# Performance work log

Measured on AMD Instinct MI355X. Metric: run time of the kernel, lower is better.

## Reference

```python
import jax, jax.numpy as jnp
import numpy as np

N_HEAD, DK, DV = 16, 64, 64
TEMP = DK ** 0.5
LN_EPS = 1e-5


def setup_inputs() -> dict:
    key = jax.random.key(0)
    ks = jax.random.split(key, 8)
    B, LQ, LK = 8, 1024, 1024
    D1, D2 = 768, 1024
    return {
        'q': jax.random.normal(ks[0], (B, LQ, D1), jnp.float32),
        'k': jax.random.normal(ks[1], (B, LK, D2), jnp.float32),
        'v': jax.random.normal(ks[2], (B, LK, D2), jnp.float32),
        'w_qs': jax.random.normal(ks[3], (D1, N_HEAD * DK), jnp.float32) * 0.02,
        'w_ks': jax.random.normal(ks[4], (D2, N_HEAD * DK), jnp.float32) * 0.02,
        'w_vs': jax.random.normal(ks[5], (D2, N_HEAD * DV), jnp.float32) * 0.02,
        'fc_w': jax.random.normal(ks[6], (N_HEAD * DV, D2), jnp.float32) * 0.02,
        'resid_w': jax.random.normal(ks[7], (D1, N_HEAD * DV), jnp.float32) * 0.02,
        'resid_b': jnp.zeros((N_HEAD * DV,), jnp.float32),
        'ln_gamma': jnp.ones((D2,), jnp.float32),
        'ln_beta': jnp.zeros((D2,), jnp.float32),
    }


def reference(q, k, v, w_qs, w_ks, w_vs, fc_w, resid_w, resid_b, ln_gamma, ln_beta):
    B, LQ, _ = q.shape
    LK = k.shape[1]
    residual = q
    # project and split heads: [B, L, H, d] -> [B, H, L, d]
    Q = (q @ w_qs).reshape(B, LQ, N_HEAD, DK).transpose(0, 2, 1, 3)
    K = (k @ w_ks).reshape(B, LK, N_HEAD, DK).transpose(0, 2, 1, 3)
    V = (v @ w_vs).reshape(B, LK, N_HEAD, DV).transpose(0, 2, 1, 3)
    scores = jnp.einsum('bhqd,bhkd->bhqk', Q / TEMP, K)
    p = jax.nn.softmax(scores, axis=-1)
    # reverse-complement attention (RCA): reverse=True
    p = (1.0 - p) / (LK - 1)
    out = jnp.einsum('bhqk,bhkd->bhqd', p, V)  # dropout is eval-mode identity
    out = out.transpose(0, 2, 1, 3).reshape(B, LQ, N_HEAD * DV)
    out = out @ fc_w
    out = out + (residual @ resid_w + resid_b)
    mean = jnp.mean(out, axis=-1, keepdims=True)
    var = jnp.var(out, axis=-1, keepdims=True)
    out = (out - mean) * jax.lax.rsqrt(var + LN_EPS) * ln_gamma + ln_beta
    return out  # relu=False
```

## Files before the change

### kernel.cpp

```cpp
#include <hip/hip_runtime.h>

typedef __bf16 bf16_t;
typedef __bf16 bf16x8 __attribute__((ext_vector_type(8)));
typedef __bf16 bf16x4 __attribute__((ext_vector_type(4)));
typedef float  f32x4  __attribute__((ext_vector_type(4)));

#if __has_builtin(__builtin_amdgcn_exp2f)
#define EXP2(x) __builtin_amdgcn_exp2f(x)
#else
#define EXP2(x) exp2f(x)
#endif

#define DEVFN __device__ __forceinline__

DEVFN void gl_lds16(void* lds_base, const void* gsrc) {
  __builtin_amdgcn_global_load_lds(
      (const __attribute__((address_space(1))) void*)gsrc,
      (__attribute__((address_space(3))) void*)lds_base, 16, 0, 0);
}

__global__ __launch_bounds__(256) void k_prep(
    const float* __restrict__ q, const float* __restrict__ k, const float* __restrict__ v,
    const float* __restrict__ w_qs, const float* __restrict__ w_ks,
    const float* __restrict__ w_vs, const float* __restrict__ fc_w,
    const float* __restrict__ resid_w,
    bf16_t* __restrict__ qb, bf16_t* __restrict__ kb, bf16_t* __restrict__ vb,
    bf16_t* __restrict__ wqsT, bf16_t* __restrict__ wksT, bf16_t* __restrict__ wvsT,
    bf16_t* __restrict__ fcwT, bf16_t* __restrict__ rswT,
    float* __restrict__ Vs) {
  __shared__ float t[64][65];
  int bid = blockIdx.x;
  if (bid < 1152) {
    const float* w; bf16_t* wt; int K;
    if (bid < 192)      { w = w_qs;    wt = wqsT; K = 768; }
    else if (bid < 448) { w = w_ks;    wt = wksT; K = 1024; bid -= 192; }
    else if (bid < 704) { w = w_vs;    wt = wvsT; K = 1024; bid -= 448; }
    else if (bid < 960) { w = fc_w;    wt = fcwT; K = 1024; bid -= 704; }
    else                { w = resid_w; wt = rswT; K = 768;  bid -= 960; }
    const int bk = (bid >> 4) << 6;
    const int bn = (bid & 15) << 6;
    const int rr = threadIdx.x >> 4;
    const int cc = (threadIdx.x & 15) << 2;
#pragma unroll
    for (int i = 0; i < 4; ++i) {
      int r = i * 16 + rr;
      float4 vv = *reinterpret_cast<const float4*>(&w[(size_t)(bk + r) * 1024 + bn + cc]);
      t[r][cc] = vv.x; t[r][cc + 1] = vv.y; t[r][cc + 2] = vv.z; t[r][cc + 3] = vv.w;
    }
    __syncthreads();
#pragma unroll
    for (int i = 0; i < 4; ++i) {
      int n = i * 16 + rr;
      bf16x4 o;
      o[0] = (bf16_t)t[cc][n];     o[1] = (bf16_t)t[cc + 1][n];
      o[2] = (bf16_t)t[cc + 2][n]; o[3] = (bf16_t)t[cc + 3][n];
      *reinterpret_cast<bf16x4*>(&wt[(size_t)(bn + n) * K + bk + cc]) = o;
    }
    return;
  }
  bid -= 1152;
  if (bid == 0) {
    for (int j = threadIdx.x; j < 8192; j += 256) Vs[j] = 0.f;
  }
  const int NQ = 1572864, NK = 2097152, NT = NQ + 2 * NK;
  int stride = (gridDim.x - 1152) * 256;
  for (int i = bid * 256 + threadIdx.x; i < NT; i += stride) {
    const float* src; bf16_t* dst; int off;
    if (i < NQ)           { src = q; dst = qb; off = i; }
    else if (i < NQ + NK) { src = k; dst = kb; off = i - NQ; }
    else                  { src = v; dst = vb; off = i - NQ - NK; }
    float4 vv = reinterpret_cast<const float4*>(src)[off];
    bf16x4 o;
    o[0] = (bf16_t)vv.x; o[1] = (bf16_t)vv.y; o[2] = (bf16_t)vv.z; o[3] = (bf16_t)vv.w;
    reinterpret_cast<bf16x4*>(dst)[off] = o;
  }
}

DEVFN void gemm_tiles(const bf16_t* __restrict__ A, const bf16_t* __restrict__ Bt,
                      int K, int m0, int n0, bf16_t (*sm)[4096], f32x4 (&acc)[4][4]) {
  const int lane = threadIdx.x & 63;
  const int wv = threadIdx.x >> 6;
  const int wr = (wv >> 1) * 64, wc = (wv & 1) * 64;
  const int lr = lane & 15, lk = lane >> 4;
  const int so0 = wv * 2048 + lane * 16;
  const int so1 = so0 + 1024;
  const int r0 = so0 >> 6, r1 = so1 >> 6;
  const int c0 = ((((so0 >> 4) & 3) ^ ((r0 >> 1) & 3)) << 4);
  const int c1 = ((((so1 >> 4) & 3) ^ ((r1 >> 1) & 3)) << 4);
  const int asw = ((lk ^ ((lr >> 1) & 3)) << 4);
  const char* Apc = (const char*)A;
  const char* Btc = (const char*)Bt;
  f32x4 zro = {0.f, 0.f, 0.f, 0.f};
#pragma unroll
  for (int i = 0; i < 4; ++i)
#pragma unroll
    for (int j = 0; j < 4; ++j) acc[i][j] = zro;

  const int nk = K >> 5;
  auto stage = [&](int buf, int t) {
    gl_lds16((char*)sm[buf] + wv * 2048,        Apc + ((size_t)(m0 + r0) * K + t * 32) * 2 + c0);
    gl_lds16((char*)sm[buf] + wv * 2048 + 1024, Apc + ((size_t)(m0 + r1) * K + t * 32) * 2 + c1);
    gl_lds16((char*)sm[2 + buf] + wv * 2048,        Btc + ((size_t)(n0 + r0) * K + t * 32) * 2 + c0);
    gl_lds16((char*)sm[2 + buf] + wv * 2048 + 1024, Btc + ((size_t)(n0 + r1) * K + t * 32) * 2 + c1);
  };
  stage(0, 0);
  __syncthreads();
  for (int t = 0; t < nk; ++t) {
    const int cur = t & 1;
    if (t + 1 < nk) stage(cur ^ 1, t + 1);
    const char* AsB = (const char*)sm[cur];
    const char* BsB = (const char*)sm[2 + cur];
    bf16x8 af[4], bfr[4];
#pragma unroll
    for (int i = 0; i < 4; ++i)
      af[i] = *(const bf16x8*)(AsB + (wr + i * 16 + lr) * 64 + asw);
#pragma unroll
    for (int j = 0; j < 4; ++j)
      bfr[j] = *(const bf16x8*)(BsB + (wc + j * 16 + lr) * 64 + asw);
#pragma unroll
    for (int i = 0; i < 4; ++i)
#pragma unroll
      for (int j = 0; j < 4; ++j)
        acc[i][j] = __builtin_amdgcn_mfma_f32_16x16x32_bf16(af[i], bfr[j], acc[i][j], 0, 0, 0);
    __syncthreads();
  }
}

__global__ __launch_bounds__(256) void k_gemm_proj(
    const bf16_t* __restrict__ qb, const bf16_t* __restrict__ wqsT, bf16_t* __restrict__ Qp,
    const bf16_t* __restrict__ kb, const bf16_t* __restrict__ wksT, bf16_t* __restrict__ Kp,
    const bf16_t* __restrict__ vb, const bf16_t* __restrict__ wvsT, bf16_t* __restrict__ Vt,
    float* __restrict__ Vsum, float qscale) {
  __shared__ bf16_t sm[4][4096];
  const int bid = blockIdx.x;
  const int route = bid >> 9;
  const int sbid = bid & 511;
  const int wg = (sbid & 7) * 64 + (sbid >> 3);
  const int tn = 8;
  const int m0 = (wg / tn) << 7;
  const int n0 = (wg % tn) << 7;
  const int lane = threadIdx.x & 63;
  const int wv = threadIdx.x >> 6;
  const int wr = (wv >> 1) * 64, wc = (wv & 1) * 64;
  const int lr = lane & 15, lk = lane >> 4;
  f32x4 acc[4][4];

  if (route == 0) {
    gemm_tiles(vb, wvsT, 1024, m0, n0, sm, acc);
    const int b = m0 >> 10;
    const int h0 = n0 >> 6;
    const int kt0 = (m0 & 1023) >> 6;
    const int h_local = wc >> 6, kt_local = wr >> 6;
    char* tl = (char*)sm + (h_local * 2 + kt_local) * 8192;
#pragma unroll
    for (int i = 0; i < 4; ++i) {
      const int kvl = i * 16 + lk * 4;
      const int csel = kvl >> 3;
      const int hoff = (kvl & 7) * 2;
#pragma unroll
      for (int j = 0; j < 4; ++j) {
        const int d = j * 16 + lr;
        bf16x4 pw;
#pragma unroll
        for (int r = 0; r < 4; ++r) pw[r] = (bf16_t)acc[i][j][r];
        *reinterpret_cast<bf16x4*>(tl + d * 128 + ((csel ^ (d & 7)) << 4) + hoff) = pw;
      }
    }
    {
      const size_t gbase = (size_t)(b * 16 + h0 + h_local) * 131072 +
                           (size_t)(kt0 + kt_local) * 8192;
#pragma unroll
      for (int it = 0; it < 8; ++it)
        *reinterpret_cast<uint4*>((char*)Vt + gbase + it * 1024 + lane * 16) =
            *reinterpret_cast<const uint4*>(tl + it * 1024 + lane * 16);
    }
    const int h = h0 + h_local;
#pragma unroll
    for (int j = 0; j < 4; ++j) {
      float s = 0.f;
#pragma unroll
      for (int i = 0; i < 4; ++i)
#pragma unroll
        for (int r = 0; r < 4; ++r) s += acc[i][j][r];
      s += __shfl_xor(s, 16, 64);
      s += __shfl_xor(s, 32, 64);
      if (lane < 16)
        atomicAdd(&Vsum[(b * 16 + h) * 64 + j * 16 + lane], s);
    }
  } else if (route == 1) {
    gemm_tiles(kb, wksT, 1024, m0, n0, sm, acc);
#pragma unroll
    for (int i = 0; i < 4; ++i)
#pragma unroll
      for (int j = 0; j < 4; ++j)
#pragma unroll
        for (int r = 0; r < 4; ++r)
          Kp[(size_t)(m0 + wr + i * 16 + lk * 4 + r) * 1024 + n0 + wc + j * 16 + lr] =
              (bf16_t)acc[i][j][r];
  } else {
    gemm_tiles(qb, wqsT, 768, m0, n0, sm, acc);
#pragma unroll
    for (int i = 0; i < 4; ++i)
#pragma unroll
      for (int j = 0; j < 4; ++j)
#pragma unroll
        for (int r = 0; r < 4; ++r)
          Qp[(size_t)(m0 + wr + i * 16 + lk * 4 + r) * 1024 + n0 + wc + j * 16 + lr] =
              (bf16_t)(acc[i][j][r] * qscale);
  }
}

__global__ __launch_bounds__(256) void k_gemm_final(
    const bf16_t* __restrict__ A1, const bf16_t* __restrict__ B1t, int K1,
    const bf16_t* __restrict__ A2, const bf16_t* __restrict__ B2t, int K2,
    const float* __restrict__ bias, bf16_t* __restrict__ Y, int N) {
  __shared__ bf16_t sm[4][4096];
  const int bpx = gridDim.x >> 3;
  const int wg = (blockIdx.x & 7) * bpx + (blockIdx.x >> 3);
  const int tn = N >> 7;
  const int m0 = (wg / tn) << 7;
  const int n0 = (wg % tn) << 7;
  const int lane = threadIdx.x & 63;
  const int wv = threadIdx.x >> 6;
  const int wr = (wv >> 1) * 64, wc = (wv & 1) * 64;
  const int lr = lane & 15, lk = lane >> 4;
  const int so0 = wv * 2048 + lane * 16;
  const int so1 = so0 + 1024;
  const int r0 = so0 >> 6, r1 = so1 >> 6;
  const int c0 = ((((so0 >> 4) & 3) ^ ((r0 >> 1) & 3)) << 4);
  const int c1 = ((((so1 >> 4) & 3) ^ ((r1 >> 1) & 3)) << 4);
  const int asw = ((lk ^ ((lr >> 1) & 3)) << 4);
  f32x4 zro = {0.f, 0.f, 0.f, 0.f};
  f32x4 acc[4][4];
#pragma unroll
  for (int i = 0; i < 4; ++i)
#pragma unroll
    for (int j = 0; j < 4; ++j) acc[i][j] = zro;

  const int nk1 = K1 >> 5;
  const int nkt = (K1 + K2) >> 5;
  auto stage = [&](int buf, int t) {
    const char* Apc; const char* Btc; int K, tt;
    if (t < nk1) { Apc = (const char*)A1; Btc = (const char*)B1t; K = K1; tt = t; }
    else         { Apc = (const char*)A2; Btc = (const char*)B2t; K = K2; tt = t - nk1; }
    gl_lds16((char*)sm[buf] + wv * 2048,        Apc + ((size_t)(m0 + r0) * K + tt * 32) * 2 + c0);
    gl_lds16((char*)sm[buf] + wv * 2048 + 1024, Apc + ((size_t)(m0 + r1) * K + tt * 32) * 2 + c1);
    gl_lds16((char*)sm[2 + buf] + wv * 2048,        Btc + ((size_t)(n0 + r0) * K + tt * 32) * 2 + c0);
    gl_lds16((char*)sm[2 + buf] + wv * 2048 + 1024, Btc + ((size_t)(n0 + r1) * K + tt * 32) * 2 + c1);
  };
  stage(0, 0);
  __syncthreads();
  for (int t = 0; t < nkt; ++t) {
    const int cur = t & 1;
    if (t + 1 < nkt) stage(cur ^ 1, t + 1);
    const char* AsB = (const char*)sm[cur];
    const char* BsB = (const char*)sm[2 + cur];
    bf16x8 af[4], bfr[4];
#pragma unroll
    for (int i = 0; i < 4; ++i)
      af[i] = *(const bf16x8*)(AsB + (wr + i * 16 + lr) * 64 + asw);
#pragma unroll
    for (int j = 0; j < 4; ++j)
      bfr[j] = *(const bf16x8*)(BsB + (wc + j * 16 + lr) * 64 + asw);
#pragma unroll
    for (int i = 0; i < 4; ++i)
#pragma unroll
      for (int j = 0; j < 4; ++j)
        acc[i][j] = __builtin_amdgcn_mfma_f32_16x16x32_bf16(af[i], bfr[j], acc[i][j], 0, 0, 0);
    __syncthreads();
  }
#pragma unroll
  for (int i = 0; i < 4; ++i)
#pragma unroll
    for (int j = 0; j < 4; ++j) {
      float bv = bias[n0 + wc + j * 16 + lr];
#pragma unroll
      for (int r = 0; r < 4; ++r)
        Y[(size_t)(m0 + wr + i * 16 + lk * 4 + r) * N + n0 + wc + j * 16 + lr] =
            (bf16_t)(acc[i][j][r] + bv);
    }
}

__global__ __launch_bounds__(1024) void k_attn(
    const bf16_t* __restrict__ Qp, const bf16_t* __restrict__ Kp,
    const bf16_t* __restrict__ Vt, const float* __restrict__ Vsum,
    bf16_t* __restrict__ Aout) {
  const int bid = blockIdx.x;
  const int wgid = (bid & 7) * 32 + (bid >> 3);
  const int qg = wgid & 1;
  const int bh = wgid >> 1;
  const int b = bh >> 4, h = bh & 15;
  __shared__ bf16_t Ks[2][4096];
  __shared__ bf16_t Vs[2][4096];
  const int tid = threadIdx.x;
  const int lane = tid & 63;
  const int wv = tid >> 6;
  const int lr = lane & 15, lk = lane >> 4;
  const int stb = (wv >> 2) * 2;
  const int wrow = (wv & 3) * 16;

  const int o = (tid & 511) * 16;
  const int row = o >> 7;
  const int sc = ((((o >> 4) & 7) ^ (row & 7)) << 4);
  const int srow = (row & 0x23) | ((row & 0x0C) << 1) | ((row & 0x10) >> 2);
  const bool isK = tid < 512;

  const char* Ksrc  = (const char*)(Kp + ((size_t)(b * 1024 + srow)) * 1024 + h * 64) + sc;
  const char* Vtile = (const char*)Vt + (size_t)bh * 131072 + o;
  const char* gsrc   = isK ? Ksrc : Vtile;
  const size_t gstep = isK ? (size_t)131072 : (size_t)8192;
  char* l0 = isK ? ((char*)&Ks[0][0] + o) : ((char*)&Vs[0][0] + o);
  char* l1 = isK ? ((char*)&Ks[1][0] + o) : ((char*)&Vs[1][0] + o);

  gl_lds16(l0, gsrc);

  bf16x8 qa[2][2];
#pragma unroll
  for (int stl = 0; stl < 2; ++stl) {
    const char* qsrc = (const char*)(Qp +
        ((size_t)(b * 1024 + qg * 512 + (stb + stl) * 64 + wrow + lr)) * 1024 + h * 64);
    qa[stl][0] = *(const bf16x8*)(qsrc + lk * 16);
    qa[stl][1] = *(const bf16x8*)(qsrc + 64 + lk * 16);
  }
  __syncthreads();

  const int kb0 = lr * 128 + ((lk ^ (lr & 7)) << 4);
  const int kb1 = lr * 128 + (((4 + lk) ^ (lr & 7)) << 4);

  f32x4 zro = {0.f, 0.f, 0.f, 0.f};
  f32x4 oacc[2][4];
  f32x4 sum[2];
#pragma unroll
  for (int stl = 0; stl < 2; ++stl) {
    sum[stl] = zro;
#pragma unroll
    for (int g = 0; g < 4; ++g) oacc[stl][g] = zro;
  }
  bf16x8 ones8;
#pragma unroll
  for (int j = 0; j < 8; ++j) ones8[j] = (bf16_t)1.0f;

  for (int kt = 0; kt < 16; ++kt) {
    const int cur = kt & 1;
    const char* KsB = (const char*)&Ks[cur][0];
    const char* VsB = (const char*)&Vs[cur][0];
    if (kt < 15)
      gl_lds16(cur ? l0 : l1, gsrc + (size_t)(kt + 1) * gstep);

    f32x4 sacc[2][4];
#pragma unroll
    for (int stl = 0; stl < 2; ++stl)
#pragma unroll
      for (int g = 0; g < 4; ++g) sacc[stl][g] = zro;
    {
      bf16x8 kf[4];
#pragma unroll
      for (int g = 0; g < 4; ++g) kf[g] = *(const bf16x8*)(KsB + kb0 + g * 2048);
#pragma unroll
      for (int stl = 0; stl < 2; ++stl)
#pragma unroll
        for (int g = 0; g < 4; ++g)
          sacc[stl][g] = __builtin_amdgcn_mfma_f32_16x16x32_bf16(kf[g], qa[stl][0], sacc[stl][g], 0, 0, 0);
#pragma unroll
      for (int g = 0; g < 4; ++g) kf[g] = *(const bf16x8*)(KsB + kb1 + g * 2048);
#pragma unroll
      for (int stl = 0; stl < 2; ++stl)
#pragma unroll
        for (int g = 0; g < 4; ++g)
          sacc[stl][g] = __builtin_amdgcn_mfma_f32_16x16x32_bf16(kf[g], qa[stl][1], sacc[stl][g], 0, 0, 0);
    }

    bf16x8 pa[2][2];
#pragma unroll
    for (int stl = 0; stl < 2; ++stl)
#pragma unroll
      for (int c = 0; c < 2; ++c) {
        bf16x8 pw;
#pragma unroll
        for (int r = 0; r < 4; ++r) {
          pw[r]     = (bf16_t)EXP2(sacc[stl][2 * c][r]);
          pw[4 + r] = (bf16_t)EXP2(sacc[stl][2 * c + 1][r]);
        }
        pa[stl][c] = pw;
      }

#pragma unroll
    for (int c = 0; c < 2; ++c) {
      const int vb = (c == 0) ? kb0 : kb1;
      bf16x8 vf[4];
#pragma unroll
      for (int gd = 0; gd < 4; ++gd)
        vf[gd] = *(const bf16x8*)(VsB + vb + gd * 2048);
#pragma unroll
      for (int stl = 0; stl < 2; ++stl) {
        sum[stl] = __builtin_amdgcn_mfma_f32_16x16x32_bf16(pa[stl][c], ones8, sum[stl], 0, 0, 0);
#pragma unroll
        for (int gd = 0; gd < 4; ++gd)
          oacc[stl][gd] = __builtin_amdgcn_mfma_f32_16x16x32_bf16(pa[stl][c], vf[gd], oacc[stl][gd], 0, 0, 0);
      }
    }
    __syncthreads();
  }

  float vs_d[4];
#pragma unroll
  for (int gd = 0; gd < 4; ++gd) vs_d[gd] = Vsum[bh * 64 + gd * 16 + lr];
#pragma unroll
  for (int stl = 0; stl < 2; ++stl) {
    float inv[4];
#pragma unroll
    for (int r = 0; r < 4; ++r) inv[r] = 1.0f / sum[stl][r];
#pragma unroll
    for (int gd = 0; gd < 4; ++gd)
#pragma unroll
      for (int r = 0; r < 4; ++r) {
        int d = gd * 16 + lr;
        int qrow = qg * 512 + (stb + stl) * 64 + wrow + lk * 4 + r;
        float attnv = oacc[stl][gd][r] * inv[r];
        float val = (vs_d[gd] - attnv) * (1.0f / 1023.0f);
        Aout[((size_t)(b * 1024 + qrow)) * 1024 + h * 64 + d] = (bf16_t)val;
      }
  }
}

__global__ __launch_bounds__(256) void k_ln(
    const bf16_t* __restrict__ Y, const float* __restrict__ gamma,
    const float* __restrict__ beta, float* __restrict__ out) {
  const int row = blockIdx.x, tid = threadIdx.x;
  bf16x4 xv = reinterpret_cast<const bf16x4*>(Y + (size_t)row * 1024)[tid];
  float x0 = (float)xv[0], x1 = (float)xv[1], x2 = (float)xv[2], x3 = (float)xv[3];
  float s = x0 + x1 + x2 + x3;
  float q = x0 * x0 + x1 * x1 + x2 * x2 + x3 * x3;
#pragma unroll
  for (int off = 32; off > 0; off >>= 1) {
    s += __shfl_xor(s, off, 64);
    q += __shfl_xor(q, off, 64);
  }
  __shared__ float ss[4], qs[4];
  if ((tid & 63) == 0) { ss[tid >> 6] = s; qs[tid >> 6] = q; }
  __syncthreads();
  s = ss[0] + ss[1] + ss[2] + ss[3];
  q = qs[0] + qs[1] + qs[2] + qs[3];
  float mean = s * (1.f / 1024.f);
  float var = q * (1.f / 1024.f) - mean * mean;
  float rstd = rsqrtf(var + 1e-5f);
  float4 g = reinterpret_cast<const float4*>(gamma)[tid];
  float4 bt = reinterpret_cast<const float4*>(beta)[tid];
  float4 o;
  o.x = (x0 - mean) * rstd * g.x + bt.x;
  o.y = (x1 - mean) * rstd * g.y + bt.y;
  o.z = (x2 - mean) * rstd * g.z + bt.z;
  o.w = (x3 - mean) * rstd * g.w + bt.w;
  reinterpret_cast<float4*>(out + (size_t)row * 1024)[tid] = o;
}

extern "C" void kernel_launch(void* const* d_in, const int* in_sizes, int n_in,
                              void* d_out, int out_size, void* d_ws, size_t ws_size,
                              hipStream_t stream) {
  (void)in_sizes; (void)n_in; (void)out_size;
  const float* q       = (const float*)d_in[0];
  const float* k       = (const float*)d_in[1];
  const float* v       = (const float*)d_in[2];
  const float* w_qs    = (const float*)d_in[3];
  const float* w_ks    = (const float*)d_in[4];
  const float* w_vs    = (const float*)d_in[5];
  const float* fc_w    = (const float*)d_in[6];
  const float* resid_w = (const float*)d_in[7];
  const float* resid_b = (const float*)d_in[8];
  const float* ln_g    = (const float*)d_in[9];
  const float* ln_b    = (const float*)d_in[10];
  float* out = (float*)d_out;
  char* ws = (char*)d_ws;

  if (ws_size < (size_t)122716160) return;

  bf16_t* qb   = (bf16_t*)(ws + 0);
  bf16_t* kb   = (bf16_t*)(ws + 12582912);
  bf16_t* vb   = (bf16_t*)(ws + 29360128);
  bf16_t* Y    = (bf16_t*)(ws + 12582912);
  bf16_t* wqsT = (bf16_t*)(ws + 46137344);
  bf16_t* wksT = (bf16_t*)(ws + 47710208);
  bf16_t* wvsT = (bf16_t*)(ws + 49807360);
  bf16_t* fcwT = (bf16_t*)(ws + 51904512);
  bf16_t* rswT = (bf16_t*)(ws + 54001664);
  bf16_t* Qp   = (bf16_t*)(ws + 55574528);
  bf16_t* Kp   = (bf16_t*)(ws + 72351744);
  bf16_t* Aout = (bf16_t*)(ws + 89128960);
  bf16_t* VtT  = (bf16_t*)(ws + 105906176);
  float*  Vsm  = (float*)(ws + 122683392);

  k_prep<<<3200, 256, 0, stream>>>(q, k, v, w_qs, w_ks, w_vs, fc_w, resid_w,
                                   qb, kb, vb, wqsT, wksT, wvsT, fcwT, rswT, Vsm);
  k_gemm_proj<<<1536, 256, 0, stream>>>(qb, wqsT, Qp, kb, wksT, Kp, vb, wvsT, VtT,
                                        Vsm, 0.18033688011f);
  k_attn<<<256, 1024, 0, stream>>>(Qp, Kp, VtT, Vsm, Aout);
  k_gemm_final<<<512, 256, 0, stream>>>(Aout, fcwT, 1024, qb, rswT, 768, resid_b, Y, 1024);
  k_ln<<<8192, 256, 0, stream>>>(Y, ln_g, ln_b, out);
}
```

Before: 177.8 us.

## Triple-buffer GEMM LDS staging with explicit vmcnt waits and raw barriers

Both projection and final GEMMs move from double-buffered to triple-buffered LDS staging, keeping two tiles of global-to-LDS loads in flight. Explicit s_waitcnt vmcnt counters and raw s_barrier replace __syncthreads, so a wave waits only for the oldest tile instead of draining every outstanding load. LDS per block grows from 32KB to 48KB and launch bounds request 3 blocks per CU. This can lower occupancy, and the hand-written vmcnt accounting and barrier placement risk ordering bugs.

```diff
diff --git a/kernel.cpp b/kernel.cpp
--- a/kernel.cpp
+++ b/kernel.cpp
@@ -98,18 +98,24 @@
 
   const int nk = K >> 5;
   auto stage = [&](int buf, int t) {
-    gl_lds16((char*)sm[buf] + wv * 2048,        Apc + ((size_t)(m0 + r0) * K + t * 32) * 2 + c0);
-    gl_lds16((char*)sm[buf] + wv * 2048 + 1024, Apc + ((size_t)(m0 + r1) * K + t * 32) * 2 + c1);
-    gl_lds16((char*)sm[2 + buf] + wv * 2048,        Btc + ((size_t)(n0 + r0) * K + t * 32) * 2 + c0);
-    gl_lds16((char*)sm[2 + buf] + wv * 2048 + 1024, Btc + ((size_t)(n0 + r1) * K + t * 32) * 2 + c1);
+    gl_lds16((char*)sm[2 * buf]     + wv * 2048,        Apc + ((size_t)(m0 + r0) * K + t * 32) * 2 + c0);
+    gl_lds16((char*)sm[2 * buf]     + wv * 2048 + 1024, Apc + ((size_t)(m0 + r1) * K + t * 32) * 2 + c1);
+    gl_lds16((char*)sm[2 * buf + 1] + wv * 2048,        Btc + ((size_t)(n0 + r0) * K + t * 32) * 2 + c0);
+    gl_lds16((char*)sm[2 * buf + 1] + wv * 2048 + 1024, Btc + ((size_t)(n0 + r1) * K + t * 32) * 2 + c1);
   };
   stage(0, 0);
-  __syncthreads();
+  if (nk > 1) {
+    stage(1, 1);
+    asm volatile("s_waitcnt vmcnt(4)" ::: "memory");
+  } else {
+    asm volatile("s_waitcnt vmcnt(0)" ::: "memory");
+  }
+  __builtin_amdgcn_s_barrier();
+
   for (int t = 0; t < nk; ++t) {
-    const int cur = t & 1;
-    if (t + 1 < nk) stage(cur ^ 1, t + 1);
-    const char* AsB = (const char*)sm[cur];
-    const char* BsB = (const char*)sm[2 + cur];
+    const int cur = t % 3;
+    const char* AsB = (const char*)sm[2 * cur];
+    const char* BsB = (const char*)sm[2 * cur + 1];
     bf16x8 af[4], bfr[4];
 #pragma unroll
     for (int i = 0; i < 4; ++i)
@@ -122,16 +128,22 @@
 #pragma unroll
       for (int j = 0; j < 4; ++j)
         acc[i][j] = __builtin_amdgcn_mfma_f32_16x16x32_bf16(af[i], bfr[j], acc[i][j], 0, 0, 0);
-    __syncthreads();
-  }
-}
-
-__global__ __launch_bounds__(256) void k_gemm_proj(
+    __builtin_amdgcn_s_barrier();
+    if (t + 2 < nk) stage((t + 2) % 3, t + 2);
+    if (t + 1 < nk) {
+      if (t + 2 < nk) asm volatile("s_waitcnt vmcnt(4)" ::: "memory");
+      else            asm volatile("s_waitcnt vmcnt(0)" ::: "memory");
+      __builtin_amdgcn_s_barrier();
+    }
+  }
+}
+
+__global__ __launch_bounds__(256, 3) void k_gemm_proj(
     const bf16_t* __restrict__ qb, const bf16_t* __restrict__ wqsT, bf16_t* __restrict__ Qp,
     const bf16_t* __restrict__ kb, const bf16_t* __restrict__ wksT, bf16_t* __restrict__ Kp,
     const bf16_t* __restrict__ vb, const bf16_t* __restrict__ wvsT, bf16_t* __restrict__ Vt,
     float* __restrict__ Vsum, float qscale) {
-  __shared__ bf16_t sm[4][4096];
+  __shared__ bf16_t sm[6][4096];
   const int bid = blockIdx.x;
   const int route = bid >> 9;
   const int sbid = bid & 511;
@@ -210,11 +222,11 @@
   }
 }
 
-__global__ __launch_bounds__(256) void k_gemm_final(
+__global__ __launch_bounds__(256, 3) void k_gemm_final(
     const bf16_t* __restrict__ A1, const bf16_t* __restrict__ B1t, int K1,
     const bf16_t* __restrict__ A2, const bf16_t* __restrict__ B2t, int K2,
     const float* __restrict__ bias, bf16_t* __restrict__ Y, int N) {
-  __shared__ bf16_t sm[4][4096];
+  __shared__ bf16_t sm[6][4096];
   const int bpx = gridDim.x >> 3;
   const int wg = (blockIdx.x & 7) * bpx + (blockIdx.x >> 3);
   const int tn = N >> 7;
@@ -243,18 +255,19 @@
     const char* Apc; const char* Btc; int K, tt;
     if (t < nk1) { Apc = (const char*)A1; Btc = (const char*)B1t; K = K1; tt = t; }
     else         { Apc = (const char*)A2; Btc = (const char*)B2t; K = K2; tt = t - nk1; }
-    gl_lds16((char*)sm[buf] + wv * 2048,        Apc + ((size_t)(m0 + r0) * K + tt * 32) * 2 + c0);
-    gl_lds16((char*)sm[buf] + wv * 2048 + 1024, Apc + ((size_t)(m0 + r1) * K + tt * 32) * 2 + c1);
-    gl_lds16((char*)sm[2 + buf] + wv * 2048,        Btc + ((size_t)(n0 + r0) * K + tt * 32) * 2 + c0);
-    gl_lds16((char*)sm[2 + buf] + wv * 2048 + 1024, Btc + ((size_t)(n0 + r1) * K + tt * 32) * 2 + c1);
+    gl_lds16((char*)sm[2 * buf]     + wv * 2048,        Apc + ((size_t)(m0 + r0) * K + tt * 32) * 2 + c0);
+    gl_lds16((char*)sm[2 * buf]     + wv * 2048 + 1024, Apc + ((size_t)(m0 + r1) * K + tt * 32) * 2 + c1);
+    gl_lds16((char*)sm[2 * buf + 1] + wv * 2048,        Btc + ((size_t)(n0 + r0) * K + tt * 32) * 2 + c0);
+    gl_lds16((char*)sm[2 * buf + 1] + wv * 2048 + 1024, Btc + ((size_t)(n0 + r1) * K + tt * 32) * 2 + c1);
   };
   stage(0, 0);
-  __syncthreads();
+  stage(1, 1);
+  asm volatile("s_waitcnt vmcnt(4)" ::: "memory");
+  __builtin_amdgcn_s_barrier();
   for (int t = 0; t < nkt; ++t) {
-    const int cur = t & 1;
-    if (t + 1 < nkt) stage(cur ^ 1, t + 1);
-    const char* AsB = (const char*)sm[cur];
-    const char* BsB = (const char*)sm[2 + cur];
+    const int cur = t % 3;
+    const char* AsB = (const char*)sm[2 * cur];
+    const char* BsB = (const char*)sm[2 * cur + 1];
     bf16x8 af[4], bfr[4];
 #pragma unroll
     for (int i = 0; i < 4; ++i)
@@ -267,7 +280,13 @@
 #pragma unroll
       for (int j = 0; j < 4; ++j)
         acc[i][j] = __builtin_amdgcn_mfma_f32_16x16x32_bf16(af[i], bfr[j], acc[i][j], 0, 0, 0);
-    __syncthreads();
+    __builtin_amdgcn_s_barrier();
+    if (t + 2 < nkt) stage((t + 2) % 3, t + 2);
+    if (t + 1 < nkt) {
+      if (t + 2 < nkt) asm volatile("s_waitcnt vmcnt(4)" ::: "memory");
+      else             asm volatile("s_waitcnt vmcnt(0)" ::: "memory");
+      __builtin_amdgcn_s_barrier();
+    }
   }
 #pragma unroll
   for (int i = 0; i < 4; ++i)
```

Result: faster. 168.1 us (median of 3 runs) (-5.4%).
